# Kernel tuning notes

Hardware: AMD Instinct MI355X
Metric: run time of the kernel (lower is better)

## Reference

```python
import jax, jax.numpy as jnp
import numpy as np

N_NODES = 100000
N_EDGES = 3200000


def gcn_conv(x, edge_index, W, b, num_nodes):
    """PyG GCNConv: x' = D^{-1/2} (A + I) D^{-1/2} (x W) + b (symmetric norm, self-loops)."""
    x = x @ W  # [N, out]
    loop = jnp.arange(num_nodes, dtype=edge_index.dtype)
    src = jnp.concatenate([edge_index[0], loop])
    dst = jnp.concatenate([edge_index[1], loop])
    # degree over destination nodes (incl. self loops)
    deg = jax.ops.segment_sum(jnp.ones_like(dst, dtype=x.dtype), dst, num_segments=num_nodes)
    dinv = jnp.where(deg > 0, jax.lax.rsqrt(deg), 0.0)
    norm = dinv[src] * dinv[dst]  # [E + N]
    msg = x[src] * norm[:, None]  # gather + scale
    out = jax.ops.segment_sum(msg, dst, num_segments=num_nodes)  # scatter-add
    return out + b


def setup_inputs() -> dict:
    key = jax.random.key(0)
    k = jax.random.split(key, 5)
    x = jax.random.normal(k[0], (N_NODES, 256), dtype=jnp.float32)
    edge_index = jax.random.randint(k[1], (2, N_EDGES), 0, N_NODES, dtype=jnp.int64)
    W1 = jax.random.normal(k[2], (256, 16), dtype=jnp.float32) * (1.0 / np.sqrt(256))
    b1 = jnp.zeros((16,), dtype=jnp.float32)
    W2 = jax.random.normal(k[3], (16, 8), dtype=jnp.float32) * (1.0 / np.sqrt(16))
    b2 = jnp.zeros((8,), dtype=jnp.float32)
    return {"x": x, "edge_index": edge_index, "W1": W1, "b1": b1, "W2": W2, "b2": b2}


def reference(x, edge_index, W1, b1, W2, b2):
    n = x.shape[0]
    h = gcn_conv(x, edge_index, W1, b1, n)
    h = jax.nn.relu(h)
    # dropout is identity in eval mode (training=False)
    h = gcn_conv(h, edge_index, W2, b2, n)
    return jax.nn.log_softmax(h, axis=1)
```

## Files before the change

### kernel.cpp

```cpp
#include <hip/hip_runtime.h>

#define NN 100000
#define NE 3200000
#define NB 391
#define CAP 9216
#define PB 16
#define CH_A (256 * PB)

__device__ __forceinline__ float4 f4add(float4 a, float4 b) {
  return make_float4(a.x + b.x, a.y + b.y, a.z + b.z, a.w + b.w);
}
__device__ __forceinline__ float4 f4fma(float s, float4 a, float4 c) {
  c.x = fmaf(s, a.x, c.x); c.y = fmaf(s, a.y, c.y);
  c.z = fmaf(s, a.z, c.z); c.w = fmaf(s, a.w, c.w);
  return c;
}

template<int CTRL>
__device__ __forceinline__ float4 quad_bcast(float4 v) {
  float4 r;
  r.x = __int_as_float(__builtin_amdgcn_update_dpp(__float_as_int(v.x), __float_as_int(v.x), CTRL, 0xF, 0xF, false));
  r.y = __int_as_float(__builtin_amdgcn_update_dpp(__float_as_int(v.y), __float_as_int(v.y), CTRL, 0xF, 0xF, false));
  r.z = __int_as_float(__builtin_amdgcn_update_dpp(__float_as_int(v.z), __float_as_int(v.z), CTRL, 0xF, 0xF, false));
  r.w = __int_as_float(__builtin_amdgcn_update_dpp(__float_as_int(v.w), __float_as_int(v.w), CTRL, 0xF, 0xF, false));
  return r;
}

__device__ __forceinline__ int edge_val(const int* __restrict__ ei, int idx, bool w64) {
  return w64 ? ei[2 * idx] : ei[idx];
}

__global__ void detect_kernel(const int* __restrict__ ei, int* __restrict__ flag) {
  if (threadIdx.x == 0 && blockIdx.x == 0) {
    int o = 0;
    for (int i = 1; i < 64; i += 2) o |= ei[i];
    *flag = (o == 0) ? 1 : 0;
  }
}

__global__ __launch_bounds__(256) void bin_kernel(const int* __restrict__ ei,
                                                  int* __restrict__ bucket_cursor,
                                                  int* __restrict__ pairs,
                                                  const int* __restrict__ flag) {
  __shared__ int  cnt[4][NB];
  __shared__ int  wcur[4][NB];
  __shared__ int  lbase[NB];
  __shared__ int  gbase[NB];
  __shared__ int  sc[512];
  __shared__ int2 stage[CH_A];
  int t = threadIdx.x;
  int wv = t >> 6;
  for (int k = t; k < 4 * NB; k += 256) (&cnt[0][0])[k] = 0;
  __syncthreads();
  bool w64 = (*flag != 0);
  int base = blockIdx.x * CH_A;
  int nval = min(CH_A, NE - base);
  int s[PB], d[PB];
#pragma unroll
  for (int i = 0; i < PB; ++i) {
    int e = base + i * 256 + t;
    if (e < NE) {
      s[i] = edge_val(ei, e, w64);
      d[i] = edge_val(ei, NE + e, w64);
      atomicAdd(&cnt[wv][d[i] >> 8], 1);
    } else {
      d[i] = -1;
    }
  }
  __syncthreads();
  int tA = (t < NB) ? cnt[0][t] + cnt[1][t] + cnt[2][t] + cnt[3][t] : 0;
  int tB = (t + 256 < NB) ? cnt[0][t + 256] + cnt[1][t + 256] + cnt[2][t + 256] + cnt[3][t + 256] : 0;
  sc[t] = tA; sc[t + 256] = tB;
  __syncthreads();
#pragma unroll
  for (int off = 1; off < 512; off <<= 1) {
    int u0 = (t >= off) ? sc[t - off] : 0;
    int u1 = (t + 256 >= off) ? sc[t + 256 - off] : 0;
    __syncthreads();
    sc[t] += u0; sc[t + 256] += u1;
    __syncthreads();
  }
#pragma unroll
  for (int h = 0; h < 2; ++h) {
    int k = t + h * 256;
    if (k < NB) {
      int tot = (h == 0) ? tA : tB;
      int lb = sc[k] - tot;
      lbase[k] = lb;
      gbase[k] = (tot > 0) ? atomicAdd(&bucket_cursor[k], tot) : 0;
      int c0 = cnt[0][k], c1 = cnt[1][k], c2 = cnt[2][k];
      wcur[0][k] = lb;
      wcur[1][k] = lb + c0;
      wcur[2][k] = lb + c0 + c1;
      wcur[3][k] = lb + c0 + c1 + c2;
    }
  }
  __syncthreads();
#pragma unroll
  for (int i = 0; i < PB; ++i) {
    if (d[i] >= 0) {
      int b = d[i] >> 8;
      int slot = atomicAdd(&wcur[wv][b], 1);
      stage[slot] = make_int2(s[i], d[i]);
    }
  }
  __syncthreads();
  for (int k = t; k < nval; k += 256) {
    int2 p = stage[k];
    int b = p.y >> 8;
    pairs[(size_t)b * CAP + gbase[b] + (k - lbase[b])] = p.x | ((p.y & 255) << 24);
  }
}

__global__ __launch_bounds__(256) void bscan_kernel(const int* __restrict__ bucket_cursor,
                                                    int* __restrict__ bucket_scan) {
  __shared__ int sc[512];
  __shared__ int orig[512];
  int t = threadIdx.x;
  int v0 = (t < NB) ? bucket_cursor[t] : 0;
  int v1 = (t + 256 < NB) ? bucket_cursor[t + 256] : 0;
  sc[t] = v0; orig[t] = v0;
  sc[t + 256] = v1; orig[t + 256] = v1;
  __syncthreads();
#pragma unroll
  for (int off = 1; off < 512; off <<= 1) {
    int u0 = (t >= off) ? sc[t - off] : 0;
    int u1 = (t + 256 >= off) ? sc[t + 256 - off] : 0;
    __syncthreads();
    sc[t] += u0; sc[t + 256] += u1;
    __syncthreads();
  }
  if (t < NB) bucket_scan[t] = sc[t] - orig[t];
  if (t + 256 < NB) bucket_scan[t + 256] = sc[t + 256] - orig[t + 256];
}

__global__ __launch_bounds__(512) void sort_kernel(const int* __restrict__ pairs,
                                                   const int* __restrict__ bucket_cursor,
                                                   const int* __restrict__ bucket_scan,
                                                   int* __restrict__ srt,
                                                   int* __restrict__ deg,
                                                   int* __restrict__ row_ofs,
                                                   float* __restrict__ dinv) {
  __shared__ int hist[256];
  __shared__ int sc[256];
  __shared__ int cur[256];
  int t = threadIdx.x;
  int b = blockIdx.x;
  int cnt_b = bucket_cursor[b];
  size_t in_base = (size_t)b * CAP;
  int out_base = bucket_scan[b];
  if (t < 256) hist[t] = 0;
  __syncthreads();
  for (int i = t; i < cnt_b; i += 512) {
    int pk = pairs[in_base + i];
    atomicAdd(&hist[((unsigned)pk) >> 24], 1);
  }
  __syncthreads();
  if (t < 256) sc[t] = hist[t];
  __syncthreads();
#pragma unroll
  for (int off = 1; off < 256; off <<= 1) {
    int u = (t < 256 && t >= off) ? sc[t - off] : 0;
    __syncthreads();
    if (t < 256) sc[t] += u;
    __syncthreads();
  }
  if (t < 256) {
    int excl = sc[t] - hist[t];
    cur[t] = out_base + excl;
    int n = b * 256 + t;
    if (n < NN) {
      deg[n] = hist[t];
      row_ofs[n] = out_base + excl;
      dinv[n] = rsqrtf((float)hist[t] + 1.0f);
    }
  }
  __syncthreads();
  for (int i = t; i < cnt_b; i += 512) {
    int pk = pairs[in_base + i];
    int pos = atomicAdd(&cur[((unsigned)pk) >> 24], 1);
    srt[pos] = pk & 0xFFFFFF;
  }
}

__global__ __launch_bounds__(256) void gemm1_kernel(const float* __restrict__ x,
                                                    const float* __restrict__ W1,
                                                    const float* __restrict__ dinv,
                                                    float* __restrict__ xw1s) {
  const int lane = threadIdx.x & 63;
  const int wv   = threadIdx.x >> 6;
  const int node0 = (blockIdx.x * 4 + wv) * 8;
  const int cg = lane >> 2;
  const int jl = lane & 3;
  float4 w[16];
#pragma unroll
  for (int k = 0; k < 4; ++k)
#pragma unroll
    for (int c = 0; c < 4; ++c)
      w[k * 4 + c] = *(const float4*)(W1 + (cg * 16 + k * 4 + c) * 16 + jl * 4);
  float4 xv[8];
#pragma unroll
  for (int i = 0; i < 8; ++i)
    xv[i] = *(const float4*)(x + (size_t)(node0 + i) * 256 + lane * 4);
  float4 acc[8];
#pragma unroll
  for (int i = 0; i < 8; ++i) acc[i] = make_float4(0.f, 0.f, 0.f, 0.f);
#pragma unroll
  for (int i = 0; i < 8; ++i) {
    float4 b = quad_bcast<0x00>(xv[i]);
    acc[i] = f4fma(b.x, w[0], acc[i]);  acc[i] = f4fma(b.y, w[1], acc[i]);
    acc[i] = f4fma(b.z, w[2], acc[i]);  acc[i] = f4fma(b.w, w[3], acc[i]);
  }
#pragma unroll
  for (int i = 0; i < 8; ++i) {
    float4 b = quad_bcast<0x55>(xv[i]);
    acc[i] = f4fma(b.x, w[4], acc[i]);  acc[i] = f4fma(b.y, w[5], acc[i]);
    acc[i] = f4fma(b.z, w[6], acc[i]);  acc[i] = f4fma(b.w, w[7], acc[i]);
  }
#pragma unroll
  for (int i = 0; i < 8; ++i) {
    float4 b = quad_bcast<0xAA>(xv[i]);
    acc[i] = f4fma(b.x, w[8], acc[i]);  acc[i] = f4fma(b.y, w[9], acc[i]);
    acc[i] = f4fma(b.z, w[10], acc[i]); acc[i] = f4fma(b.w, w[11], acc[i]);
  }
#pragma unroll
  for (int i = 0; i < 8; ++i) {
    float4 b = quad_bcast<0xFF>(xv[i]);
    acc[i] = f4fma(b.x, w[12], acc[i]); acc[i] = f4fma(b.y, w[13], acc[i]);
    acc[i] = f4fma(b.z, w[14], acc[i]); acc[i] = f4fma(b.w, w[15], acc[i]);
  }
#pragma unroll
  for (int m = 4; m <= 32; m <<= 1) {
#pragma unroll
    for (int i = 0; i < 8; ++i) {
      acc[i].x += __shfl_xor(acc[i].x, m);
      acc[i].y += __shfl_xor(acc[i].y, m);
      acc[i].z += __shfl_xor(acc[i].z, m);
      acc[i].w += __shfl_xor(acc[i].w, m);
    }
  }
  if (lane < 4) {
#pragma unroll
    for (int i = 0; i < 8; ++i) {
      float dn = dinv[node0 + i];
      float4 a = acc[i];
      a.x *= dn; a.y *= dn; a.z *= dn; a.w *= dn;
      *(float4*)(xw1s + (node0 + i) * 16 + lane * 4) = a;
    }
  }
}

__global__ __launch_bounds__(256) void layer1_kernel(const int* __restrict__ srt,
                                                     const int* __restrict__ row_ofs,
                                                     const int* __restrict__ deg,
                                                     const float* __restrict__ dinv,
                                                     const float* __restrict__ xw1s,
                                                     const float* __restrict__ W2,
                                                     const float* __restrict__ b1,
                                                     float* __restrict__ h1w2s) {
  int t = blockIdx.x * 256 + threadIdx.x;
  int n = t >> 4, sub = t & 15, q = sub & 3, e = sub >> 2;
  if (n >= NN) return;
  int base = row_ofs[n], cnt = deg[n];
  float4 acc = make_float4(0.f, 0.f, 0.f, 0.f);
  int s_next = (e < cnt) ? srt[base + e] : 0;
  for (int i = e; i < cnt; i += 4) {
    int s = s_next;
    if (i + 4 < cnt) s_next = srt[base + i + 4];
    acc = f4add(acc, *(const float4*)(xw1s + s * 16 + q * 4));
  }
#pragma unroll
  for (int m = 4; m <= 8; m <<= 1) {
    acc.x += __shfl_xor(acc.x, m);
    acc.y += __shfl_xor(acc.y, m);
    acc.z += __shfl_xor(acc.z, m);
    acc.w += __shfl_xor(acc.w, m);
  }
  float dn = dinv[n];
  float4 sv = *(const float4*)(xw1s + n * 16 + q * 4);
  float4 bv = *(const float4*)(b1 + q * 4);
  float h[4];
  h[0] = fmaxf(fmaf(dn, acc.x + sv.x, bv.x), 0.f);
  h[1] = fmaxf(fmaf(dn, acc.y + sv.y, bv.y), 0.f);
  h[2] = fmaxf(fmaf(dn, acc.z + sv.z, bv.z), 0.f);
  h[3] = fmaxf(fmaf(dn, acc.w + sv.w, bv.w), 0.f);
  float p[8] = {0.f, 0.f, 0.f, 0.f, 0.f, 0.f, 0.f, 0.f};
  const float4* W2v = (const float4*)W2;
#pragma unroll
  for (int f = 0; f < 4; ++f) {
    float4 wlo = W2v[(q * 4 + f) * 2];
    float4 whi = W2v[(q * 4 + f) * 2 + 1];
    p[0] = fmaf(h[f], wlo.x, p[0]); p[1] = fmaf(h[f], wlo.y, p[1]);
    p[2] = fmaf(h[f], wlo.z, p[2]); p[3] = fmaf(h[f], wlo.w, p[3]);
    p[4] = fmaf(h[f], whi.x, p[4]); p[5] = fmaf(h[f], whi.y, p[5]);
    p[6] = fmaf(h[f], whi.z, p[6]); p[7] = fmaf(h[f], whi.w, p[7]);
  }
#pragma unroll
  for (int m = 1; m <= 2; m <<= 1)
#pragma unroll
    for (int j = 0; j < 8; ++j)
      p[j] += __shfl_xor(p[j], m);
  if (sub == 0)
    *(float4*)(h1w2s + n * 8) = make_float4(dn * p[0], dn * p[1], dn * p[2], dn * p[3]);
  else if (sub == 1)
    *(float4*)(h1w2s + n * 8 + 4) = make_float4(dn * p[4], dn * p[5], dn * p[6], dn * p[7]);
}

__global__ __launch_bounds__(256) void layer2_kernel(const int* __restrict__ srt,
                                                     const int* __restrict__ row_ofs,
                                                     const int* __restrict__ deg,
                                                     const float* __restrict__ dinv,
                                                     const float* __restrict__ h1w2s,
                                                     const float* __restrict__ b2,
                                                     float* __restrict__ out) {
  int t = blockIdx.x * 256 + threadIdx.x;
  int n = t >> 3, sub = t & 7, q = sub & 1, e = sub >> 1;
  if (n >= NN) return;
  int base = row_ofs[n], cnt = deg[n];
  float4 acc = make_float4(0.f, 0.f, 0.f, 0.f);
  int s_next = (e < cnt) ? srt[base + e] : 0;
  for (int i = e; i < cnt; i += 4) {
    int s = s_next;
    if (i + 4 < cnt) s_next = srt[base + i + 4];
    acc = f4add(acc, *(const float4*)(h1w2s + s * 8 + q * 4));
  }
#pragma unroll
  for (int m = 2; m <= 4; m <<= 1) {
    acc.x += __shfl_xor(acc.x, m);
    acc.y += __shfl_xor(acc.y, m);
    acc.z += __shfl_xor(acc.z, m);
    acc.w += __shfl_xor(acc.w, m);
  }
  float dn = dinv[n];
  float4 sv = *(const float4*)(h1w2s + n * 8 + q * 4);
  float4 bv = *(const float4*)(b2 + q * 4);
  float4 v;
  v.x = fmaf(dn, acc.x + sv.x, bv.x);
  v.y = fmaf(dn, acc.y + sv.y, bv.y);
  v.z = fmaf(dn, acc.z + sv.z, bv.z);
  v.w = fmaf(dn, acc.w + sv.w, bv.w);
  float mh = fmaxf(fmaxf(v.x, v.y), fmaxf(v.z, v.w));
  float m = fmaxf(mh, __shfl_xor(mh, 1));
  float se = expf(v.x - m) + expf(v.y - m) + expf(v.z - m) + expf(v.w - m);
  float st = se + __shfl_xor(se, 1);
  float ls = m + logf(st);
  if (sub < 2)
    *(float4*)(out + n * 8 + q * 4) = make_float4(v.x - ls, v.y - ls, v.z - ls, v.w - ls);
}

extern "C" void kernel_launch(void* const* d_in, const int* in_sizes, int n_in,
                              void* d_out, int out_size, void* d_ws, size_t ws_size,
                              hipStream_t stream) {
  const float* x  = (const float*)d_in[0];
  const int*   ei = (const int*)d_in[1];
  const float* W1 = (const float*)d_in[2];
  const float* b1 = (const float*)d_in[3];
  const float* W2 = (const float*)d_in[4];
  const float* b2 = (const float*)d_in[5];
  float* out = (float*)d_out;

  const size_t region0_bytes = (size_t)NB * CAP * sizeof(int);
  int*   pairs   = (int*)d_ws;
  float* xw1s    = (float*)d_ws;
  float* h1w2s   = xw1s + (size_t)16 * NN;
  float* dinv    = (float*)((char*)d_ws + region0_bytes);
  int*   deg     = (int*)(dinv + NN);
  int*   row_ofs = deg + NN;
  int*   srt     = row_ofs + NN;
  int*   bucket_cursor = srt + NE;
  int*   bucket_scan   = bucket_cursor + NB + 1;
  int*   flag          = bucket_scan + NB + 1;

  hipMemsetAsync(bucket_cursor, 0, NB * sizeof(int), stream);
  detect_kernel<<<1, 64, 0, stream>>>(ei, flag);
  bin_kernel<<<(NE + CH_A - 1) / CH_A, 256, 0, stream>>>(ei, bucket_cursor, pairs, flag);
  bscan_kernel<<<1, 256, 0, stream>>>(bucket_cursor, bucket_scan);
  sort_kernel<<<NB, 512, 0, stream>>>(pairs, bucket_cursor, bucket_scan, srt, deg, row_ofs, dinv);
  gemm1_kernel<<<NN / 32, 256, 0, stream>>>(x, W1, dinv, xw1s);
  layer1_kernel<<<(16 * NN + 255) / 256, 256, 0, stream>>>(srt, row_ofs, deg, dinv, xw1s, W2, b1, h1w2s);
  layer2_kernel<<<(8 * NN + 255) / 256, 256, 0, stream>>>(srt, row_ofs, deg, dinv, h1w2s, b2, out);
}
```

Baseline: 330.8 us.

## Aggregate per destination bucket in LDS, drop CSR sort, store features as fp16

```diff
diff --git a/kernel.cpp b/kernel.cpp
--- a/kernel.cpp
+++ b/kernel.cpp
@@ -7,9 +7,9 @@
 #define PB 16
 #define CH_A (256 * PB)
 
-__device__ __forceinline__ float4 f4add(float4 a, float4 b) {
-  return make_float4(a.x + b.x, a.y + b.y, a.z + b.z, a.w + b.w);
-}
+typedef _Float16 half4 __attribute__((ext_vector_type(4)));
+typedef _Float16 half8 __attribute__((ext_vector_type(8)));
+
 __device__ __forceinline__ float4 f4fma(float s, float4 a, float4 c) {
   c.x = fmaf(s, a.x, c.x); c.y = fmaf(s, a.y, c.y);
   c.z = fmaf(s, a.z, c.z); c.w = fmaf(s, a.w, c.w);
@@ -30,8 +30,12 @@
   return w64 ? ei[2 * idx] : ei[idx];
 }
 
-__global__ void detect_kernel(const int* __restrict__ ei, int* __restrict__ flag) {
-  if (threadIdx.x == 0 && blockIdx.x == 0) {
+__global__ __launch_bounds__(512) void init_kernel(const int* __restrict__ ei,
+                                                   int* __restrict__ bucket_cursor,
+                                                   int* __restrict__ flag) {
+  int t = threadIdx.x;
+  if (t < NB) bucket_cursor[t] = 0;
+  if (t == 511) {
     int o = 0;
     for (int i = 1; i < 64; i += 2) o |= ei[i];
     *flag = (o == 0) ? 1 : 0;
@@ -112,81 +116,27 @@
   }
 }
 
-__global__ __launch_bounds__(256) void bscan_kernel(const int* __restrict__ bucket_cursor,
-                                                    int* __restrict__ bucket_scan) {
-  __shared__ int sc[512];
-  __shared__ int orig[512];
-  int t = threadIdx.x;
-  int v0 = (t < NB) ? bucket_cursor[t] : 0;
-  int v1 = (t + 256 < NB) ? bucket_cursor[t + 256] : 0;
-  sc[t] = v0; orig[t] = v0;
-  sc[t + 256] = v1; orig[t + 256] = v1;
-  __syncthreads();
-#pragma unroll
-  for (int off = 1; off < 512; off <<= 1) {
-    int u0 = (t >= off) ? sc[t - off] : 0;
-    int u1 = (t + 256 >= off) ? sc[t + 256 - off] : 0;
-    __syncthreads();
-    sc[t] += u0; sc[t + 256] += u1;
-    __syncthreads();
-  }
-  if (t < NB) bucket_scan[t] = sc[t] - orig[t];
-  if (t + 256 < NB) bucket_scan[t + 256] = sc[t + 256] - orig[t + 256];
-}
-
-__global__ __launch_bounds__(512) void sort_kernel(const int* __restrict__ pairs,
-                                                   const int* __restrict__ bucket_cursor,
-                                                   const int* __restrict__ bucket_scan,
-                                                   int* __restrict__ srt,
-                                                   int* __restrict__ deg,
-                                                   int* __restrict__ row_ofs,
-                                                   float* __restrict__ dinv) {
+__global__ __launch_bounds__(256) void degscan_kernel(const int* __restrict__ pairs,
+                                                      const int* __restrict__ bucket_cursor,
+                                                      float* __restrict__ dinv) {
   __shared__ int hist[256];
-  __shared__ int sc[256];
-  __shared__ int cur[256];
   int t = threadIdx.x;
   int b = blockIdx.x;
   int cnt_b = bucket_cursor[b];
   size_t in_base = (size_t)b * CAP;
-  int out_base = bucket_scan[b];
-  if (t < 256) hist[t] = 0;
-  __syncthreads();
-  for (int i = t; i < cnt_b; i += 512) {
-    int pk = pairs[in_base + i];
-    atomicAdd(&hist[((unsigned)pk) >> 24], 1);
-  }
-  __syncthreads();
-  if (t < 256) sc[t] = hist[t];
-  __syncthreads();
-#pragma unroll
-  for (int off = 1; off < 256; off <<= 1) {
-    int u = (t < 256 && t >= off) ? sc[t - off] : 0;
-    __syncthreads();
-    if (t < 256) sc[t] += u;
-    __syncthreads();
-  }
-  if (t < 256) {
-    int excl = sc[t] - hist[t];
-    cur[t] = out_base + excl;
-    int n = b * 256 + t;
-    if (n < NN) {
-      deg[n] = hist[t];
-      row_ofs[n] = out_base + excl;
-      dinv[n] = rsqrtf((float)hist[t] + 1.0f);
-    }
-  }
-  __syncthreads();
-  for (int i = t; i < cnt_b; i += 512) {
-    int pk = pairs[in_base + i];
-    int pos = atomicAdd(&cur[((unsigned)pk) >> 24], 1);
-    srt[pos] = pk & 0xFFFFFF;
-  }
+  hist[t] = 0;
+  __syncthreads();
+  for (int i = t; i < cnt_b; i += 256)
+    atomicAdd(&hist[((unsigned)pairs[in_base + i]) >> 24], 1);
+  __syncthreads();
+  int n = b * 256 + t;
+  if (n < NN) dinv[n] = rsqrtf((float)hist[t] + 1.0f);
 }
 
 __global__ __launch_bounds__(256) void gemm1_kernel(const float* __restrict__ x,
                                                     const float* __restrict__ W1,
                                                     const float* __restrict__ dinv,
-                                                    float* __restrict__ xw1s) {
+                                                    _Float16* __restrict__ xw1h) {
   const int lane = threadIdx.x & 63;
   const int wv   = threadIdx.x >> 6;
   const int node0 = (blockIdx.x * 4 + wv) * 8;
@@ -244,108 +194,114 @@
     for (int i = 0; i < 8; ++i) {
       float dn = dinv[node0 + i];
       float4 a = acc[i];
-      a.x *= dn; a.y *= dn; a.z *= dn; a.w *= dn;
-      *(float4*)(xw1s + (node0 + i) * 16 + lane * 4) = a;
-    }
-  }
-}
-
-__global__ __launch_bounds__(256) void layer1_kernel(const int* __restrict__ srt,
-                                                     const int* __restrict__ row_ofs,
-                                                     const int* __restrict__ deg,
+      half4 hv;
+      hv[0] = (_Float16)(a.x * dn); hv[1] = (_Float16)(a.y * dn);
+      hv[2] = (_Float16)(a.z * dn); hv[3] = (_Float16)(a.w * dn);
+      *(half4*)(xw1h + (size_t)(node0 + i) * 16 + lane * 4) = hv;
+    }
+  }
+}
+
+#define A1S 17
+__global__ __launch_bounds__(512) void layer1_kernel(const int* __restrict__ pairs,
+                                                     const int* __restrict__ bucket_cursor,
                                                      const float* __restrict__ dinv,
-                                                     const float* __restrict__ xw1s,
+                                                     const _Float16* __restrict__ xw1h,
                                                      const float* __restrict__ W2,
                                                      const float* __restrict__ b1,
-                                                     float* __restrict__ h1w2s) {
-  int t = blockIdx.x * 256 + threadIdx.x;
-  int n = t >> 4, sub = t & 15, q = sub & 3, e = sub >> 2;
+                                                     _Float16* __restrict__ h1w2h) {
+  __shared__ float agg[256 * A1S];
+  int t = threadIdx.x;
+  int b = blockIdx.x;
+  int cnt_b = bucket_cursor[b];
+  size_t in_base = (size_t)b * CAP;
+  for (int k = t; k < 256 * A1S; k += 512) agg[k] = 0.f;
+  __syncthreads();
+  int q = t & 3;
+  for (int i = t >> 2; i < cnt_b; i += 128) {
+    int pk = pairs[in_base + i];
+    int s = pk & 0xFFFFFF;
+    int dl = ((unsigned)pk) >> 24;
+    half4 v = *(const half4*)(xw1h + (size_t)s * 16 + q * 4);
+    float* ap = agg + dl * A1S + q * 4;
+    atomicAdd(ap + 0, (float)v[0]);
+    atomicAdd(ap + 1, (float)v[1]);
+    atomicAdd(ap + 2, (float)v[2]);
+    atomicAdd(ap + 3, (float)v[3]);
+  }
+  __syncthreads();
+  int nl = t >> 1, hh = t & 1;
+  int n = b * 256 + nl;
   if (n >= NN) return;
-  int base = row_ofs[n], cnt = deg[n];
-  float4 acc = make_float4(0.f, 0.f, 0.f, 0.f);
-  int s_next = (e < cnt) ? srt[base + e] : 0;
-  for (int i = e; i < cnt; i += 4) {
-    int s = s_next;
-    if (i + 4 < cnt) s_next = srt[base + i + 4];
-    acc = f4add(acc, *(const float4*)(xw1s + s * 16 + q * 4));
-  }
-#pragma unroll
-  for (int m = 4; m <= 8; m <<= 1) {
-    acc.x += __shfl_xor(acc.x, m);
-    acc.y += __shfl_xor(acc.y, m);
-    acc.z += __shfl_xor(acc.z, m);
-    acc.w += __shfl_xor(acc.w, m);
-  }
   float dn = dinv[n];
-  float4 sv = *(const float4*)(xw1s + n * 16 + q * 4);
-  float4 bv = *(const float4*)(b1 + q * 4);
-  float h[4];
-  h[0] = fmaxf(fmaf(dn, acc.x + sv.x, bv.x), 0.f);
-  h[1] = fmaxf(fmaf(dn, acc.y + sv.y, bv.y), 0.f);
-  h[2] = fmaxf(fmaf(dn, acc.z + sv.z, bv.z), 0.f);
-  h[3] = fmaxf(fmaf(dn, acc.w + sv.w, bv.w), 0.f);
+  half8 svh = *(const half8*)(xw1h + (size_t)n * 16 + hh * 8);
   float p[8] = {0.f, 0.f, 0.f, 0.f, 0.f, 0.f, 0.f, 0.f};
-  const float4* W2v = (const float4*)W2;
-#pragma unroll
-  for (int f = 0; f < 4; ++f) {
-    float4 wlo = W2v[(q * 4 + f) * 2];
-    float4 whi = W2v[(q * 4 + f) * 2 + 1];
-    p[0] = fmaf(h[f], wlo.x, p[0]); p[1] = fmaf(h[f], wlo.y, p[1]);
-    p[2] = fmaf(h[f], wlo.z, p[2]); p[3] = fmaf(h[f], wlo.w, p[3]);
-    p[4] = fmaf(h[f], whi.x, p[4]); p[5] = fmaf(h[f], whi.y, p[5]);
-    p[6] = fmaf(h[f], whi.z, p[6]); p[7] = fmaf(h[f], whi.w, p[7]);
-  }
-#pragma unroll
-  for (int m = 1; m <= 2; m <<= 1)
-#pragma unroll
-    for (int j = 0; j < 8; ++j)
-      p[j] += __shfl_xor(p[j], m);
-  if (sub == 0)
-    *(float4*)(h1w2s + n * 8) = make_float4(dn * p[0], dn * p[1], dn * p[2], dn * p[3]);
-  else if (sub == 1)
-    *(float4*)(h1w2s + n * 8 + 4) = make_float4(dn * p[4], dn * p[5], dn * p[6], dn * p[7]);
-}
-
-__global__ __launch_bounds__(256) void layer2_kernel(const int* __restrict__ srt,
-                                                     const int* __restrict__ row_ofs,
-                                                     const int* __restrict__ deg,
+#pragma unroll
+  for (int f8 = 0; f8 < 8; ++f8) {
+    int f = hh * 8 + f8;
+    float hv = fmaxf(fmaf(dn, agg[nl * A1S + f] + (float)svh[f8], b1[f]), 0.f);
+    const float4* W2v = (const float4*)(W2 + f * 8);
+    float4 wlo = W2v[0], whi = W2v[1];
+    p[0] = fmaf(hv, wlo.x, p[0]); p[1] = fmaf(hv, wlo.y, p[1]);
+    p[2] = fmaf(hv, wlo.z, p[2]); p[3] = fmaf(hv, wlo.w, p[3]);
+    p[4] = fmaf(hv, whi.x, p[4]); p[5] = fmaf(hv, whi.y, p[5]);
+    p[6] = fmaf(hv, whi.z, p[6]); p[7] = fmaf(hv, whi.w, p[7]);
+  }
+#pragma unroll
+  for (int j = 0; j < 8; ++j) p[j] += __shfl_xor(p[j], 1);
+  if (hh == 0) {
+    half8 hv;
+#pragma unroll
+    for (int j = 0; j < 8; ++j) hv[j] = (_Float16)(p[j] * dn);
+    *(half8*)(h1w2h + (size_t)n * 8) = hv;
+  }
+}
+
+#define A2S 9
+__global__ __launch_bounds__(512) void layer2_kernel(const int* __restrict__ pairs,
+                                                     const int* __restrict__ bucket_cursor,
                                                      const float* __restrict__ dinv,
-                                                     const float* __restrict__ h1w2s,
+                                                     const _Float16* __restrict__ h1w2h,
                                                      const float* __restrict__ b2,
                                                      float* __restrict__ out) {
-  int t = blockIdx.x * 256 + threadIdx.x;
-  int n = t >> 3, sub = t & 7, q = sub & 1, e = sub >> 1;
+  __shared__ float agg[256 * A2S];
+  int t = threadIdx.x;
+  int b = blockIdx.x;
+  int cnt_b = bucket_cursor[b];
+  size_t in_base = (size_t)b * CAP;
+  for (int k = t; k < 256 * A2S; k += 512) agg[k] = 0.f;
+  __syncthreads();
+  int q = t & 1;
+  for (int i = t >> 1; i < cnt_b; i += 256) {
+    int pk = pairs[in_base + i];
+    int s = pk & 0xFFFFFF;
+    int dl = ((unsigned)pk) >> 24;
+    half4 v = *(const half4*)(h1w2h + (size_t)s * 8 + q * 4);
+    float* ap = agg + dl * A2S + q * 4;
+    atomicAdd(ap + 0, (float)v[0]);
+    atomicAdd(ap + 1, (float)v[1]);
+    atomicAdd(ap + 2, (float)v[2]);
+    atomicAdd(ap + 3, (float)v[3]);
+  }
+  __syncthreads();
+  if (t >= 256) return;
+  int n = b * 256 + t;
   if (n >= NN) return;
-  int base = row_ofs[n], cnt = deg[n];
-  float4 acc = make_float4(0.f, 0.f, 0.f, 0.f);
-  int s_next = (e < cnt) ? srt[base + e] : 0;
-  for (int i = e; i < cnt; i += 4) {
-    int s = s_next;
-    if (i + 4 < cnt) s_next = srt[base + i + 4];
-    acc = f4add(acc, *(const float4*)(h1w2s + s * 8 + q * 4));
-  }
-#pragma unroll
-  for (int m = 2; m <= 4; m <<= 1) {
-    acc.x += __shfl_xor(acc.x, m);
-    acc.y += __shfl_xor(acc.y, m);
-    acc.z += __shfl_xor(acc.z, m);
-    acc.w += __shfl_xor(acc.w, m);
-  }
   float dn = dinv[n];
-  float4 sv = *(const float4*)(h1w2s + n * 8 + q * 4);
-  float4 bv = *(const float4*)(b2 + q * 4);
-  float4 v;
-  v.x = fmaf(dn, acc.x + sv.x, bv.x);
-  v.y = fmaf(dn, acc.y + sv.y, bv.y);
-  v.z = fmaf(dn, acc.z + sv.z, bv.z);
-  v.w = fmaf(dn, acc.w + sv.w, bv.w);
-  float mh = fmaxf(fmaxf(v.x, v.y), fmaxf(v.z, v.w));
-  float m = fmaxf(mh, __shfl_xor(mh, 1));
-  float se = expf(v.x - m) + expf(v.y - m) + expf(v.z - m) + expf(v.w - m);
-  float st = se + __shfl_xor(se, 1);
-  float ls = m + logf(st);
-  if (sub < 2)
-    *(float4*)(out + n * 8 + q * 4) = make_float4(v.x - ls, v.y - ls, v.z - ls, v.w - ls);
+  half8 svh = *(const half8*)(h1w2h + (size_t)n * 8);
+  float v[8];
+#pragma unroll
+  for (int j = 0; j < 8; ++j)
+    v[j] = fmaf(dn, agg[t * A2S + j] + (float)svh[j], b2[j]);
+  float m = v[0];
+#pragma unroll
+  for (int j = 1; j < 8; ++j) m = fmaxf(m, v[j]);
+  float sum = 0.f;
+#pragma unroll
+  for (int j = 0; j < 8; ++j) sum += expf(v[j] - m);
+  float ls = m + logf(sum);
+  *(float4*)(out + (size_t)n * 8)     = make_float4(v[0] - ls, v[1] - ls, v[2] - ls, v[3] - ls);
+  *(float4*)(out + (size_t)n * 8 + 4) = make_float4(v[4] - ls, v[5] - ls, v[6] - ls, v[7] - ls);
 }
 
 extern "C" void kernel_launch(void* const* d_in, const int* in_sizes, int n_in,
@@ -359,24 +315,17 @@
   const float* b2 = (const float*)d_in[5];
   float* out = (float*)d_out;
 
-  const size_t region0_bytes = (size_t)NB * CAP * sizeof(int);
-  int*   pairs   = (int*)d_ws;
-  float* xw1s    = (float*)d_ws;
-  float* h1w2s   = xw1s + (size_t)16 * NN;
-  float* dinv    = (float*)((char*)d_ws + region0_bytes);
-  int*   deg     = (int*)(dinv + NN);
-  int*   row_ofs = deg + NN;
-  int*   srt     = row_ofs + NN;
-  int*   bucket_cursor = srt + NE;
-  int*   bucket_scan   = bucket_cursor + NB + 1;
-  int*   flag          = bucket_scan + NB + 1;
-
-  hipMemsetAsync(bucket_cursor, 0, NB * sizeof(int), stream);
-  detect_kernel<<<1, 64, 0, stream>>>(ei, flag);
+  int*      pairs = (int*)d_ws;
+  _Float16* xw1h  = (_Float16*)(pairs + (size_t)NB * CAP);
+  _Float16* h1w2h = xw1h + (size_t)16 * NN;
+  float*    dinv  = (float*)(h1w2h + (size_t)8 * NN);
+  int*      bucket_cursor = (int*)(dinv + NN);
+  int*      flag  = bucket_cursor + NB;
+
+  init_kernel<<<1, 512, 0, stream>>>(ei, bucket_cursor, flag);
   bin_kernel<<<(NE + CH_A - 1) / CH_A, 256, 0, stream>>>(ei, bucket_cursor, pairs, flag);
-  bscan_kernel<<<1, 256, 0, stream>>>(bucket_cursor, bucket_scan);
-  sort_kernel<<<NB, 512, 0, stream>>>(pairs, bucket_cursor, bucket_scan, srt, deg, row_ofs, dinv);
-  gemm1_kernel<<<NN / 32, 256, 0, stream>>>(x, W1, dinv, xw1s);
-  layer1_kernel<<<(16 * NN + 255) / 256, 256, 0, stream>>>(srt, row_ofs, deg, dinv, xw1s, W2, b1, h1w2s);
-  layer2_kernel<<<(8 * NN + 255) / 256, 256, 0, stream>>>(srt, row_ofs, deg, dinv, h1w2s, b2, out);
-}
+  degscan_kernel<<<NB, 256, 0, stream>>>(pairs, bucket_cursor, dinv);
+  gemm1_kernel<<<NN / 32, 256, 0, stream>>>(x, W1, dinv, xw1h);
+  layer1_kernel<<<NB, 512, 0, stream>>>(pairs, bucket_cursor, dinv, xw1h, W2, b1, h1w2h);
+  layer2_kernel<<<NB, 512, 0, stream>>>(pairs, bucket_cursor, dinv, h1w2h, b2, out);
+}
```

After: 749.9 us. 2.27x slower.

## Store intermediate node features in fp16 and fold memset into init kernel

Applied to the files above, without the earlier changes.

```diff
diff --git a/kernel.cpp b/kernel.cpp
--- a/kernel.cpp
+++ b/kernel.cpp
@@ -7,9 +7,9 @@
 #define PB 16
 #define CH_A (256 * PB)
 
-__device__ __forceinline__ float4 f4add(float4 a, float4 b) {
-  return make_float4(a.x + b.x, a.y + b.y, a.z + b.z, a.w + b.w);
-}
+typedef _Float16 half4 __attribute__((ext_vector_type(4)));
+typedef _Float16 half8 __attribute__((ext_vector_type(8)));
+
 __device__ __forceinline__ float4 f4fma(float s, float4 a, float4 c) {
   c.x = fmaf(s, a.x, c.x); c.y = fmaf(s, a.y, c.y);
   c.z = fmaf(s, a.z, c.z); c.w = fmaf(s, a.w, c.w);
@@ -30,8 +30,12 @@
   return w64 ? ei[2 * idx] : ei[idx];
 }
 
-__global__ void detect_kernel(const int* __restrict__ ei, int* __restrict__ flag) {
-  if (threadIdx.x == 0 && blockIdx.x == 0) {
+__global__ __launch_bounds__(512) void init_kernel(const int* __restrict__ ei,
+                                                   int* __restrict__ bucket_cursor,
+                                                   int* __restrict__ flag) {
+  int t = threadIdx.x;
+  if (t < NB) bucket_cursor[t] = 0;
+  if (t == 511) {
     int o = 0;
     for (int i = 1; i < 64; i += 2) o |= ei[i];
     *flag = (o == 0) ? 1 : 0;
@@ -186,7 +190,7 @@
 __global__ __launch_bounds__(256) void gemm1_kernel(const float* __restrict__ x,
                                                     const float* __restrict__ W1,
                                                     const float* __restrict__ dinv,
-                                                    float* __restrict__ xw1s) {
+                                                    _Float16* __restrict__ xw1h) {
   const int lane = threadIdx.x & 63;
   const int wv   = threadIdx.x >> 6;
   const int node0 = (blockIdx.x * 4 + wv) * 8;
@@ -244,8 +248,10 @@
     for (int i = 0; i < 8; ++i) {
       float dn = dinv[node0 + i];
       float4 a = acc[i];
-      a.x *= dn; a.y *= dn; a.z *= dn; a.w *= dn;
-      *(float4*)(xw1s + (node0 + i) * 16 + lane * 4) = a;
+      half4 hv;
+      hv[0] = (_Float16)(a.x * dn); hv[1] = (_Float16)(a.y * dn);
+      hv[2] = (_Float16)(a.z * dn); hv[3] = (_Float16)(a.w * dn);
+      *(half4*)(xw1h + (size_t)(node0 + i) * 16 + lane * 4) = hv;
     }
   }
 }
@@ -254,10 +260,10 @@
                                                      const int* __restrict__ row_ofs,
                                                      const int* __restrict__ deg,
                                                      const float* __restrict__ dinv,
-                                                     const float* __restrict__ xw1s,
+                                                     const _Float16* __restrict__ xw1h,
                                                      const float* __restrict__ W2,
                                                      const float* __restrict__ b1,
-                                                     float* __restrict__ h1w2s) {
+                                                     _Float16* __restrict__ h1w2h) {
   int t = blockIdx.x * 256 + threadIdx.x;
   int n = t >> 4, sub = t & 15, q = sub & 3, e = sub >> 2;
   if (n >= NN) return;
@@ -267,7 +273,9 @@
   for (int i = e; i < cnt; i += 4) {
     int s = s_next;
     if (i + 4 < cnt) s_next = srt[base + i + 4];
-    acc = f4add(acc, *(const float4*)(xw1s + s * 16 + q * 4));
+    half4 v = *(const half4*)(xw1h + (size_t)s * 16 + q * 4);
+    acc.x += (float)v[0]; acc.y += (float)v[1];
+    acc.z += (float)v[2]; acc.w += (float)v[3];
   }
 #pragma unroll
   for (int m = 4; m <= 8; m <<= 1) {
@@ -277,13 +285,13 @@
     acc.w += __shfl_xor(acc.w, m);
   }
   float dn = dinv[n];
-  float4 sv = *(const float4*)(xw1s + n * 16 + q * 4);
+  half4 svh = *(const half4*)(xw1h + (size_t)n * 16 + q * 4);
   float4 bv = *(const float4*)(b1 + q * 4);
   float h[4];
-  h[0] = fmaxf(fmaf(dn, acc.x + sv.x, bv.x), 0.f);
-  h[1] = fmaxf(fmaf(dn, acc.y + sv.y, bv.y), 0.f);
-  h[2] = fmaxf(fmaf(dn, acc.z + sv.z, bv.z), 0.f);
-  h[3] = fmaxf(fmaf(dn, acc.w + sv.w, bv.w), 0.f);
+  h[0] = fmaxf(fmaf(dn, acc.x + (float)svh[0], bv.x), 0.f);
+  h[1] = fmaxf(fmaf(dn, acc.y + (float)svh[1], bv.y), 0.f);
+  h[2] = fmaxf(fmaf(dn, acc.z + (float)svh[2], bv.z), 0.f);
+  h[3] = fmaxf(fmaf(dn, acc.w + (float)svh[3], bv.w), 0.f);
   float p[8] = {0.f, 0.f, 0.f, 0.f, 0.f, 0.f, 0.f, 0.f};
   const float4* W2v = (const float4*)W2;
 #pragma unroll
@@ -300,17 +308,19 @@
 #pragma unroll
     for (int j = 0; j < 8; ++j)
       p[j] += __shfl_xor(p[j], m);
-  if (sub == 0)
-    *(float4*)(h1w2s + n * 8) = make_float4(dn * p[0], dn * p[1], dn * p[2], dn * p[3]);
-  else if (sub == 1)
-    *(float4*)(h1w2s + n * 8 + 4) = make_float4(dn * p[4], dn * p[5], dn * p[6], dn * p[7]);
+  if (sub == 0) {
+    half8 hv;
+#pragma unroll
+    for (int j = 0; j < 8; ++j) hv[j] = (_Float16)(p[j] * dn);
+    *(half8*)(h1w2h + (size_t)n * 8) = hv;
+  }
 }
 
 __global__ __launch_bounds__(256) void layer2_kernel(const int* __restrict__ srt,
                                                      const int* __restrict__ row_ofs,
                                                      const int* __restrict__ deg,
                                                      const float* __restrict__ dinv,
-                                                     const float* __restrict__ h1w2s,
+                                                     const _Float16* __restrict__ h1w2h,
                                                      const float* __restrict__ b2,
                                                      float* __restrict__ out) {
   int t = blockIdx.x * 256 + threadIdx.x;
@@ -322,7 +332,9 @@
   for (int i = e; i < cnt; i += 4) {
     int s = s_next;
     if (i + 4 < cnt) s_next = srt[base + i + 4];
-    acc = f4add(acc, *(const float4*)(h1w2s + s * 8 + q * 4));
+    half4 v = *(const half4*)(h1w2h + (size_t)s * 8 + q * 4);
+    acc.x += (float)v[0]; acc.y += (float)v[1];
+    acc.z += (float)v[2]; acc.w += (float)v[3];
   }
 #pragma unroll
   for (int m = 2; m <= 4; m <<= 1) {
@@ -332,20 +344,20 @@
     acc.w += __shfl_xor(acc.w, m);
   }
   float dn = dinv[n];
-  float4 sv = *(const float4*)(h1w2s + n * 8 + q * 4);
+  half4 svh = *(const half4*)(h1w2h + (size_t)n * 8 + q * 4);
   float4 bv = *(const float4*)(b2 + q * 4);
   float4 v;
-  v.x = fmaf(dn, acc.x + sv.x, bv.x);
-  v.y = fmaf(dn, acc.y + sv.y, bv.y);
-  v.z = fmaf(dn, acc.z + sv.z, bv.z);
-  v.w = fmaf(dn, acc.w + sv.w, bv.w);
+  v.x = fmaf(dn, acc.x + (float)svh[0], bv.x);
+  v.y = fmaf(dn, acc.y + (float)svh[1], bv.y);
+  v.z = fmaf(dn, acc.z + (float)svh[2], bv.z);
+  v.w = fmaf(dn, acc.w + (float)svh[3], bv.w);
   float mh = fmaxf(fmaxf(v.x, v.y), fmaxf(v.z, v.w));
   float m = fmaxf(mh, __shfl_xor(mh, 1));
   float se = expf(v.x - m) + expf(v.y - m) + expf(v.z - m) + expf(v.w - m);
   float st = se + __shfl_xor(se, 1);
   float ls = m + logf(st);
   if (sub < 2)
-    *(float4*)(out + n * 8 + q * 4) = make_float4(v.x - ls, v.y - ls, v.z - ls, v.w - ls);
+    *(float4*)(out + (size_t)n * 8 + q * 4) = make_float4(v.x - ls, v.y - ls, v.z - ls, v.w - ls);
 }
 
 extern "C" void kernel_launch(void* const* d_in, const int* in_sizes, int n_in,
@@ -359,24 +371,22 @@
   const float* b2 = (const float*)d_in[5];
   float* out = (float*)d_out;
 
-  const size_t region0_bytes = (size_t)NB * CAP * sizeof(int);
-  int*   pairs   = (int*)d_ws;
-  float* xw1s    = (float*)d_ws;
-  float* h1w2s   = xw1s + (size_t)16 * NN;
-  float* dinv    = (float*)((char*)d_ws + region0_bytes);
-  int*   deg     = (int*)(dinv + NN);
-  int*   row_ofs = deg + NN;
-  int*   srt     = row_ofs + NN;
-  int*   bucket_cursor = srt + NE;
-  int*   bucket_scan   = bucket_cursor + NB + 1;
-  int*   flag          = bucket_scan + NB + 1;
-
-  hipMemsetAsync(bucket_cursor, 0, NB * sizeof(int), stream);
-  detect_kernel<<<1, 64, 0, stream>>>(ei, flag);
+  int*      pairs = (int*)d_ws;
+  _Float16* xw1h  = (_Float16*)(pairs + (size_t)NB * CAP);
+  _Float16* h1w2h = xw1h + (size_t)16 * NN;
+  float*    dinv  = (float*)(h1w2h + (size_t)8 * NN);
+  int*      deg   = (int*)(dinv + NN);
+  int*      row_ofs = deg + NN;
+  int*      srt   = row_ofs + NN;
+  int*      bucket_cursor = srt + NE;
+  int*      bucket_scan   = bucket_cursor + NB + 1;
+  int*      flag          = bucket_scan + NB + 1;
+
+  init_kernel<<<1, 512, 0, stream>>>(ei, bucket_cursor, flag);
   bin_kernel<<<(NE + CH_A - 1) / CH_A, 256, 0, stream>>>(ei, bucket_cursor, pairs, flag);
   bscan_kernel<<<1, 256, 0, stream>>>(bucket_cursor, bucket_scan);
   sort_kernel<<<NB, 512, 0, stream>>>(pairs, bucket_cursor, bucket_scan, srt, deg, row_ofs, dinv);
-  gemm1_kernel<<<NN / 32, 256, 0, stream>>>(x, W1, dinv, xw1s);
-  layer1_kernel<<<(16 * NN + 255) / 256, 256, 0, stream>>>(srt, row_ofs, deg, dinv, xw1s, W2, b1, h1w2s);
-  layer2_kernel<<<(8 * NN + 255) / 256, 256, 0, stream>>>(srt, row_ofs, deg, dinv, h1w2s, b2, out);
-}
+  gemm1_kernel<<<NN / 32, 256, 0, stream>>>(x, W1, dinv, xw1h);
+  layer1_kernel<<<(16 * NN + 255) / 256, 256, 0, stream>>>(srt, row_ofs, deg, dinv, xw1h, W2, b1, h1w2h);
+  layer2_kernel<<<(8 * NN + 255) / 256, 256, 0, stream>>>(srt, row_ofs, deg, dinv, h1w2h, b2, out);
+}
```

Measured after the change: 321.1 us. -2.9%, faster.
